# Performance work log

Measured on AMD Instinct MI355X. Metric: run time of the kernel, lower is better.

The kernel has to match this reference:

```python
import jax, jax.numpy as jnp
import numpy as np

B, L, D_IN, H, C = 64, 2048, 400, 200, 32
NEG = 1e12


def setup_inputs() -> dict:
    key = jax.random.key(0)
    k1, k2, k3, k4, k5 = jax.random.split(key, 5)
    x = jax.random.normal(k1, (B, L, D_IN), dtype=jnp.float32)
    category_bias = jax.random.normal(k2, (B, L, C), dtype=jnp.float32)
    att_mask = (jax.random.uniform(k3, (B, L)) > 0.2).astype(jnp.float32)
    # glorot-uniform-ish scales
    W_proj = jax.random.normal(k4, (D_IN, H), dtype=jnp.float32) * np.float32(np.sqrt(2.0 / (D_IN + H)))
    context = jax.random.normal(k5, (C, H), dtype=jnp.float32) * np.float32(np.sqrt(2.0 / (C + H)))
    lamada = jnp.zeros((1,), dtype=jnp.float32)
    return {"x": x, "category_bias": category_bias, "att_mask": att_mask,
            "W_proj": W_proj, "context": context, "lamada": lamada}


def reference(x, category_bias, att_mask, W_proj, context, lamada):
    # proj: [B, L, H] = tanh(x @ W_proj)  (Dense, no bias)
    proj = jnp.tanh(jnp.einsum("bld,dh->blh", x, W_proj))
    # scores vs learned context vectors: [B, L, C]
    weights = jnp.einsum("blh,ch->blc", proj, context) + lamada * category_bias
    # [B, C, L]
    weights = jnp.transpose(weights, (0, 2, 1))
    # additive large-negative mask, then softmax over sequence
    weights = weights - (1.0 - att_mask[:, None, :]) * NEG
    weights = jax.nn.softmax(weights, axis=-1)
    # poly representation: [B, C, D_IN]
    return jnp.einsum("bcl,bld->bcd", weights, x)
```

## Files before the change

kernel.cpp:

```cpp
#include <hip/hip_runtime.h>
#include <cmath>
#include <cstdint>

#define B_ 64
#define L_ 2048
#define DIN 400
#define H_ 200
#define C_ 32
#define NEGBIG 1e12f
#define KC1 13
#define NT1 13
#define KC2 7
#define MT2 2
#define NLC 8

typedef _Float16 half8 __attribute__((ext_vector_type(8)));
typedef float f32x4 __attribute__((ext_vector_type(4)));
typedef unsigned int uint4v __attribute__((ext_vector_type(4)));

__device__ __align__(16) _Float16 g_wfrag[KC1 * NT1 * 512];
__device__ __align__(16) _Float16 g_cfrag[KC2 * MT2 * 512];

static __device__ __forceinline__ f32x4 mfma16(half8 a, half8 b, f32x4 c) {
  return __builtin_amdgcn_mfma_f32_16x16x32_f16(a, b, c, 0, 0, 0);
}

static __device__ __forceinline__ float fast_tanh(float v) {
  const float e = __expf(2.0f * v);
  return 1.0f - 2.0f / (e + 1.0f);
}

__global__ __launch_bounds__(64) void k_prep(const float* __restrict__ Wp,
                                             const float* __restrict__ ctx)
{
  const int lane = threadIdx.x;
  const int bid = blockIdx.x;
  if (bid < KC1 * NT1) {
    const int q = bid / NT1, nt = bid % NT1;
    const int kb = q * 32 + (lane >> 4) * 8;
    const int n  = nt * 16 + (lane & 15);
    half8 h;
#pragma unroll
    for (int j = 0; j < 8; ++j) {
      const int k = kb + j;
      const float v = (k < DIN && n < H_) ? Wp[(size_t)k * H_ + n] : 0.0f;
      h[j] = (_Float16)v;
    }
    *reinterpret_cast<half8*>(&g_wfrag[((size_t)bid << 9) + (lane << 3)]) = h;
  } else {
    const int r = bid - KC1 * NT1;
    const int c  = (r % MT2) * 16 + (lane & 15);
    const int hb = (r / MT2) * 32 + (lane >> 4) * 8;
    half8 h;
#pragma unroll
    for (int j = 0; j < 8; ++j) {
      const int hh = hb + j;
      const float v = (hh < H_) ? ctx[(size_t)c * H_ + hh] : 0.0f;
      h[j] = (_Float16)v;
    }
    *reinterpret_cast<half8*>(&g_cfrag[((size_t)r << 9) + (lane << 3)]) = h;
  }
}

__global__ __launch_bounds__(256, 4) void k_scores(
    const float* __restrict__ x,
    const float* __restrict__ cb,
    const float* __restrict__ mask,
    const float* __restrict__ lam,
    float* __restrict__ S)
{
  __shared__ half8 smemv[1792];

  const int tid  = threadIdx.x;
  const int lane = tid & 63;
  const int w    = __builtin_amdgcn_readfirstlane(tid >> 6);
  const int b    = blockIdx.y;
  const int l0   = blockIdx.x * 64;
  const int oct  = lane >> 4;

  f32x4 acc[NT1];
#pragma unroll
  for (int nt = 0; nt < NT1; ++nt) acc[nt] = f32x4{0.f, 0.f, 0.f, 0.f};

  const float* xrow =
      x + ((size_t)b * L_ + l0 + w * 16 + (lane & 15)) * DIN + oct * 8;

  for (int i = w; i < NT1; i += 4) {
    const _Float16* gp = g_wfrag + (((size_t)i) << 9) + (lane << 3);
    __builtin_amdgcn_global_load_lds(
        (const __attribute__((address_space(1))) void*)gp,
        (__attribute__((address_space(3))) void*)(smemv + i * 64),
        16, 0, 0);
  }
  __builtin_amdgcn_sched_barrier(0);
  float4 cur0 = *reinterpret_cast<const float4*>(xrow);
  float4 cur1 = *reinterpret_cast<const float4*>(xrow + 4);

#pragma unroll
  for (int q = 0; q < KC1; ++q) {
    asm volatile("s_waitcnt vmcnt(2)\n\ts_barrier" ::: "memory");

    float4 nx0 = float4{0.f, 0.f, 0.f, 0.f};
    float4 nx1 = float4{0.f, 0.f, 0.f, 0.f};
    if (q < KC1 - 1) {
      const int nb = ((q + 1) & 1) * 832;
      for (int i = w; i < NT1; i += 4) {
        const _Float16* gp =
            g_wfrag + (((size_t)((q + 1) * NT1 + i)) << 9) + (lane << 3);
        __builtin_amdgcn_global_load_lds(
            (const __attribute__((address_space(1))) void*)gp,
            (__attribute__((address_space(3))) void*)(smemv + nb + i * 64),
            16, 0, 0);
      }
      __builtin_amdgcn_sched_barrier(0);
      const int k0 = (q + 1) * 32 + oct * 8;
      if (k0 + 7 < DIN) {
        nx0 = *reinterpret_cast<const float4*>(xrow + (q + 1) * 32);
        nx1 = *reinterpret_cast<const float4*>(xrow + (q + 1) * 32 + 4);
      }
    }

    float fa[8] = {cur0.x, cur0.y, cur0.z, cur0.w,
                   cur1.x, cur1.y, cur1.z, cur1.w};
    half8 ah, al;
#pragma unroll
    for (int j = 0; j < 8; ++j) {
      const _Float16 h = (_Float16)fa[j];
      ah[j] = h;
      al[j] = (_Float16)(fa[j] - (float)h);
    }

    const int base = (q & 1) * 832;
#pragma unroll
    for (int nt = 0; nt < NT1; ++nt) {
      const half8 bh = smemv[base + nt * 64 + lane];
      acc[nt] = mfma16(ah, bh, acc[nt]);
      acc[nt] = mfma16(al, bh, acc[nt]);
    }
    cur0 = nx0;
    cur1 = nx1;
  }

  __syncthreads();
  if (lane >= 32) {
    half8 z = {};
    smemv[(24 + w) * 64 + lane] = z;
  }
  _Float16* Pp = reinterpret_cast<_Float16*>(smemv);
#pragma unroll
  for (int nt = 0; nt < NT1; ++nt) {
    const int h   = nt * 16 + (lane & 15);
    const int q2  = h >> 5;
    const int lpw = ((h >> 3) & 3) << 4;
    const int jj  = h & 7;
#pragma unroll
    for (int reg = 0; reg < 4; ++reg) {
      const int t = ((lane >> 4) << 2) + reg;
      const float p = fast_tanh(acc[nt][reg]);
      Pp[(size_t)(((q2 * 4 + w) * 64) + lpw + t) * 8 + jj] = (_Float16)p;
    }
  }

  f32x4 s0 = f32x4{0.f, 0.f, 0.f, 0.f};
  f32x4 s1 = f32x4{0.f, 0.f, 0.f, 0.f};
#pragma unroll
  for (int q2 = 0; q2 < KC2; ++q2) {
    const half8 pb = smemv[(q2 * 4 + w) * 64 + lane];
    const half8 c0 = *reinterpret_cast<const half8*>(
        g_cfrag + (((size_t)(q2 * 2)) << 9) + (lane << 3));
    const half8 c1 = *reinterpret_cast<const half8*>(
        g_cfrag + (((size_t)(q2 * 2 + 1)) << 9) + (lane << 3));
    s0 = mfma16(c0, pb, s0);
    s1 = mfma16(c1, pb, s1);
  }

  const int tok = (w << 4) | (lane & 15);
  const size_t bl = (size_t)b * L_ + l0 + tok;
  const float lamv = lam[0];
  const float mk = (1.0f - mask[bl]) * NEGBIG;
  const int cq = (lane >> 4) << 2;
  const float4 cb0 = *reinterpret_cast<const float4*>(cb + bl * C_ + cq);
  const float4 cb1 = *reinterpret_cast<const float4*>(cb + bl * C_ + 16 + cq);
  float* Sp = S + (size_t)b * C_ * L_ + l0 + tok;
  Sp[(size_t)(cq + 0) * L_] = s0[0] + lamv * cb0.x - mk;
  Sp[(size_t)(cq + 1) * L_] = s0[1] + lamv * cb0.y - mk;
  Sp[(size_t)(cq + 2) * L_] = s0[2] + lamv * cb0.z - mk;
  Sp[(size_t)(cq + 3) * L_] = s0[3] + lamv * cb0.w - mk;
  Sp[(size_t)(16 + cq + 0) * L_] = s1[0] + lamv * cb1.x - mk;
  Sp[(size_t)(16 + cq + 1) * L_] = s1[1] + lamv * cb1.y - mk;
  Sp[(size_t)(16 + cq + 2) * L_] = s1[2] + lamv * cb1.z - mk;
  Sp[(size_t)(16 + cq + 3) * L_] = s1[3] + lamv * cb1.w - mk;
}

__global__ __launch_bounds__(256) void k_softmax(float* __restrict__ S,
                                                 _Float16* __restrict__ wh)
{
  const int row = blockIdx.x;
  float* R = S + (size_t)row * L_;
  const int tid = threadIdx.x;

  float v[8];
  float m = -3.4e38f;
#pragma unroll
  for (int j = 0; j < 8; ++j) {
    v[j] = R[tid + 256 * j];
    m = fmaxf(m, v[j]);
  }
#pragma unroll
  for (int o = 32; o > 0; o >>= 1) m = fmaxf(m, __shfl_xor(m, o));

  __shared__ float red[4];
  const int wid = tid >> 6;
  if ((tid & 63) == 0) red[wid] = m;
  __syncthreads();
  m = fmaxf(fmaxf(red[0], red[1]), fmaxf(red[2], red[3]));
  __syncthreads();

  float s = 0.f;
#pragma unroll
  for (int j = 0; j < 8; ++j) {
    v[j] = __expf(v[j] - m);
    s += v[j];
  }
#pragma unroll
  for (int o = 32; o > 0; o >>= 1) s += __shfl_xor(s, o);
  if ((tid & 63) == 0) red[wid] = s;
  __syncthreads();
  s = red[0] + red[1] + red[2] + red[3];

  const float inv = 1.0f / s;
  if (wh != nullptr) {
    _Float16* whr = wh + (size_t)row * L_;
#pragma unroll
    for (int j = 0; j < 8; ++j)
      whr[tid + 256 * j] = (_Float16)(v[j] * inv);
  } else {
#pragma unroll
    for (int j = 0; j < 8; ++j) R[tid + 256 * j] = v[j] * inv;
  }
}

__global__ __launch_bounds__(512, 4) void k_out_mfma(
    const float* __restrict__ x,
    const _Float16* __restrict__ wh,
    float* __restrict__ part)
{
  __shared__ unsigned int xsw[400 * 20];
  __shared__ unsigned int ws16[32][16];

  const int tid  = threadIdx.x;
  const int lane = tid & 63;
  const int w    = __builtin_amdgcn_readfirstlane(tid >> 6);
  const int b    = blockIdx.y;
  const int kq   = blockIdx.x;
  const int l0b  = kq * (L_ / NLC);

  const int ntile0 = (w < 7) ? w * 3 : 21;
  const int NTW    = (w < 7) ? 3 : 4;

  const int n   = lane & 15;
  const int oct = lane >> 4;

  f32x4 acc[4][2];
#pragma unroll
  for (int i = 0; i < 4; ++i) {
    acc[i][0] = f32x4{0.f, 0.f, 0.f, 0.f};
    acc[i][1] = f32x4{0.f, 0.f, 0.f, 0.f};
  }

  const float* xb = x + ((size_t)b * L_ + l0b) * DIN;
  const unsigned int* whb = reinterpret_cast<const unsigned int*>(
      wh + (size_t)b * C_ * L_ + l0b);

  const int lp0 = tid / 100 * 0;
  (void)lp0;

  float4 r0[4], r1[4];
  unsigned int wreg;

#pragma unroll
  for (int s = 0; s < 4; ++s) {
    const int i = s * 512 + tid;
    if (s < 3 || i < 1600) {
      const int lp = i / 100, qd = i - lp * 100;
      const float* src = xb + (size_t)(2 * lp) * DIN + 4 * qd;
      r0[s] = *reinterpret_cast<const float4*>(src);
      r1[s] = *reinterpret_cast<const float4*>(src + DIN);
    }
  }
  wreg = whb[((size_t)(tid >> 4) * L_) / 2 + (tid & 15)];

  const int NCH = (L_ / NLC) / 32;
  for (int ch = 0; ch < NCH; ++ch) {
    __syncthreads();

#pragma unroll
    for (int s = 0; s < 4; ++s) {
      const int i = s * 512 + tid;
      if (s < 3 || i < 1600) {
        const int lp = i / 100, qd = i - lp * 100;
#pragma unroll
        for (int k = 0; k < 4; ++k) {
          const int d = 4 * qd + k;
          const int sw = ((d >> 2) ^ (d >> 4)) & 3;
          const int col = (((lp >> 2) ^ sw) << 2) | (lp & 3);
          const _Float16 h0 = (_Float16)r0[s][k];
          const _Float16 h1 = (_Float16)r1[s][k];
          unsigned int pk = (unsigned int)__builtin_bit_cast(unsigned short, h0) |
                            ((unsigned int)__builtin_bit_cast(unsigned short, h1) << 16);
          xsw[d * 20 + col] = pk;
        }
      }
    }
    ws16[tid >> 4][tid & 15] = wreg;
    __syncthreads();

    if (ch + 1 < NCH) {
      const float* xc = xb + (size_t)((ch + 1) * 32) * DIN;
#pragma unroll
      for (int s = 0; s < 4; ++s) {
        const int i = s * 512 + tid;
        if (s < 3 || i < 1600) {
          const int lp = i / 100, qd = i - lp * 100;
          const float* src = xc + (size_t)(2 * lp) * DIN + 4 * qd;
          r0[s] = *reinterpret_cast<const float4*>(src);
          r1[s] = *reinterpret_cast<const float4*>(src + DIN);
        }
      }
      wreg = whb[((size_t)(tid >> 4) * L_ + (ch + 1) * 32) / 2 + (tid & 15)];
    }

    union { uint4v u; half8 h; } a0c, a1c;
    a0c.u = *reinterpret_cast<const uint4v*>(&ws16[n][oct * 4]);
    a1c.u = *reinterpret_cast<const uint4v*>(&ws16[n + 16][oct * 4]);
    const half8 a0 = a0c.h;
    const half8 a1 = a1c.h;

#pragma unroll
    for (int nt = 0; nt < 4; ++nt) {
      if (nt < NTW) {
        const int d0 = (ntile0 + nt) * 16 + n;
        const int sw = ((d0 >> 2) ^ (d0 >> 4)) & 3;
        const half8 bh = *reinterpret_cast<const half8*>(
            &xsw[d0 * 20 + ((oct ^ sw) << 2)]);
        acc[nt][0] = mfma16(a0, bh, acc[nt][0]);
        acc[nt][1] = mfma16(a1, bh, acc[nt][1]);
      }
    }
  }

  float* pb = part + ((size_t)(b * NLC + kq) * C_) * DIN;
#pragma unroll
  for (int nt = 0; nt < 4; ++nt) {
    if (nt < NTW) {
      const int d = (ntile0 + nt) * 16 + n;
#pragma unroll
      for (int mt = 0; mt < 2; ++mt) {
#pragma unroll
        for (int reg = 0; reg < 4; ++reg) {
          const int c = mt * 16 + oct * 4 + reg;
          pb[(size_t)c * DIN + d] = acc[nt][mt][reg];
        }
      }
    }
  }
}

__global__ __launch_bounds__(256) void k_out_reduce(
    const float* __restrict__ part, float* __restrict__ out)
{
  const int idx = blockIdx.x * 256 + threadIdx.x;
  const int b = idx / (C_ * DIN / 4);
  const int r = idx - b * (C_ * DIN / 4);
  const float4* p = reinterpret_cast<const float4*>(part) +
                    (size_t)b * NLC * (C_ * DIN / 4) + r;
  float4 s = float4{0.f, 0.f, 0.f, 0.f};
#pragma unroll
  for (int lc = 0; lc < NLC; ++lc) {
    const float4 v = p[(size_t)lc * (C_ * DIN / 4)];
    s.x += v.x; s.y += v.y; s.z += v.z; s.w += v.w;
  }
  reinterpret_cast<float4*>(out)[idx] = s;
}

__global__ __launch_bounds__(256) void k_out_atomic(
    const float* __restrict__ x,
    const float* __restrict__ Wt,
    float* __restrict__ out)
{
  __shared__ float ws_s[C_][256];
  const int tid  = threadIdx.x;
  const int b    = blockIdx.y;
  const int lc0  = blockIdx.x * 256;
  const int g    = __builtin_amdgcn_readfirstlane(tid >> 6);
  const int lane = tid & 63;

  {
    const int c  = tid >> 3;
    const int lb = (tid & 7) * 32;
    const float* src = Wt + ((size_t)b * C_ + c) * L_ + lc0 + lb;
#pragma unroll
    for (int j = 0; j < 32; j += 4)
      *reinterpret_cast<float4*>(&ws_s[c][lb + j]) =
          *reinterpret_cast<const float4*>(src + j);
  }
  __syncthreads();

  float a1[8][4] = {};
  float a2[8][4] = {};
  const bool has2 = lane < 36;
  const float* xb = x + ((size_t)b * L_ + lc0) * DIN;
  const int d1 = lane * 4;
  const int d2 = 256 + lane * 4;

  for (int l = 0; l < 256; ++l) {
    const float4 xv = *reinterpret_cast<const float4*>(xb + (size_t)l * DIN + d1);
    float4 xv2 = float4{0.f, 0.f, 0.f, 0.f};
    if (has2) xv2 = *reinterpret_cast<const float4*>(xb + (size_t)l * DIN + d2);
#pragma unroll
    for (int i = 0; i < 8; ++i) {
      const float wv = ws_s[g * 8 + i][l];
      a1[i][0] = fmaf(wv, xv.x, a1[i][0]);
      a1[i][1] = fmaf(wv, xv.y, a1[i][1]);
      a1[i][2] = fmaf(wv, xv.z, a1[i][2]);
      a1[i][3] = fmaf(wv, xv.w, a1[i][3]);
      a2[i][0] = fmaf(wv, xv2.x, a2[i][0]);
      a2[i][1] = fmaf(wv, xv2.y, a2[i][1]);
      a2[i][2] = fmaf(wv, xv2.z, a2[i][2]);
      a2[i][3] = fmaf(wv, xv2.w, a2[i][3]);
    }
  }

  float* ob = out + ((size_t)b * C_ + g * 8) * DIN;
#pragma unroll
  for (int i = 0; i < 8; ++i) {
#pragma unroll
    for (int kk = 0; kk < 4; ++kk)
      atomicAdd(ob + (size_t)i * DIN + d1 + kk, a1[i][kk]);
    if (has2) {
#pragma unroll
      for (int kk = 0; kk < 4; ++kk)
        atomicAdd(ob + (size_t)i * DIN + d2 + kk, a2[i][kk]);
    }
  }
}

extern "C" void kernel_launch(void* const* d_in, const int* in_sizes, int n_in,
                              void* d_out, int out_size, void* d_ws, size_t ws_size,
                              hipStream_t stream)
{
  const float* x    = (const float*)d_in[0];
  const float* cb   = (const float*)d_in[1];
  const float* mask = (const float*)d_in[2];
  const float* Wp   = (const float*)d_in[3];
  const float* ctx  = (const float*)d_in[4];
  const float* lam  = (const float*)d_in[5];
  float* out = (float*)d_out;

  const size_t part_elems = (size_t)B_ * NLC * C_ * DIN;
  float* wsf  = (float*)d_ws;
  float* S    = wsf;
  float* part = wsf;
  _Float16* wh = (_Float16*)(wsf + part_elems);
  const size_t need = part_elems * sizeof(float) +
                      (size_t)B_ * C_ * L_ * sizeof(_Float16);

  k_prep<<<dim3(KC1 * NT1 + KC2 * MT2), 64, 0, stream>>>(Wp, ctx);
  k_scores<<<dim3(L_ / 64, B_), 256, 0, stream>>>(x, cb, mask, lam, S);

  if (ws_size >= need) {
    k_softmax<<<dim3(B_ * C_), 256, 0, stream>>>(S, wh);
    k_out_mfma<<<dim3(NLC, B_), 512, 0, stream>>>(x, wh, part);
    k_out_reduce<<<dim3(B_ * C_ * DIN / 4 / 256), 256, 0, stream>>>(part, out);
  } else {
    k_softmax<<<dim3(B_ * C_), 256, 0, stream>>>(S, nullptr);
    hipMemsetAsync(d_out, 0, (size_t)out_size * sizeof(float), stream);
    k_out_atomic<<<dim3(L_ / 256, B_), 256, 0, stream>>>(x, S, out);
  }
}
```

Baseline: 116.3 us.

## Give each k_scores wave two row tiles to reuse W fragments

```diff
diff --git a/kernel.cpp b/kernel.cpp
--- a/kernel.cpp
+++ b/kernel.cpp
@@ -62,7 +62,7 @@
   }
 }
 
-__global__ __launch_bounds__(256, 4) void k_scores(
+__global__ __launch_bounds__(128, 2) void k_scores(
     const float* __restrict__ x,
     const float* __restrict__ cb,
     const float* __restrict__ mask,
@@ -78,14 +78,17 @@
   const int l0   = blockIdx.x * 64;
   const int oct  = lane >> 4;
 
-  f32x4 acc[NT1];
-#pragma unroll
-  for (int nt = 0; nt < NT1; ++nt) acc[nt] = f32x4{0.f, 0.f, 0.f, 0.f};
-
-  const float* xrow =
-      x + ((size_t)b * L_ + l0 + w * 16 + (lane & 15)) * DIN + oct * 8;
-
-  for (int i = w; i < NT1; i += 4) {
+  f32x4 acc[2][NT1];
+#pragma unroll
+  for (int mt = 0; mt < 2; ++mt)
+#pragma unroll
+    for (int nt = 0; nt < NT1; ++nt) acc[mt][nt] = f32x4{0.f, 0.f, 0.f, 0.f};
+
+  const float* xrow0 =
+      x + ((size_t)b * L_ + l0 + w * 32 + (lane & 15)) * DIN + oct * 8;
+  const float* xrow1 = xrow0 + (size_t)16 * DIN;
+
+  for (int i = w; i < NT1; i += 2) {
     const _Float16* gp = g_wfrag + (((size_t)i) << 9) + (lane << 3);
     __builtin_amdgcn_global_load_lds(
         (const __attribute__((address_space(1))) void*)gp,
@@ -93,18 +96,22 @@
         16, 0, 0);
   }
   __builtin_amdgcn_sched_barrier(0);
-  float4 cur0 = *reinterpret_cast<const float4*>(xrow);
-  float4 cur1 = *reinterpret_cast<const float4*>(xrow + 4);
+  float4 c00 = *reinterpret_cast<const float4*>(xrow0);
+  float4 c01 = *reinterpret_cast<const float4*>(xrow0 + 4);
+  float4 c10 = *reinterpret_cast<const float4*>(xrow1);
+  float4 c11 = *reinterpret_cast<const float4*>(xrow1 + 4);
 
 #pragma unroll
   for (int q = 0; q < KC1; ++q) {
-    asm volatile("s_waitcnt vmcnt(2)\n\ts_barrier" ::: "memory");
-
-    float4 nx0 = float4{0.f, 0.f, 0.f, 0.f};
-    float4 nx1 = float4{0.f, 0.f, 0.f, 0.f};
+    asm volatile("s_waitcnt vmcnt(4)\n\ts_barrier" ::: "memory");
+
+    float4 n00 = float4{0.f, 0.f, 0.f, 0.f};
+    float4 n01 = float4{0.f, 0.f, 0.f, 0.f};
+    float4 n10 = float4{0.f, 0.f, 0.f, 0.f};
+    float4 n11 = float4{0.f, 0.f, 0.f, 0.f};
     if (q < KC1 - 1) {
       const int nb = ((q + 1) & 1) * 832;
-      for (int i = w; i < NT1; i += 4) {
+      for (int i = w; i < NT1; i += 2) {
         const _Float16* gp =
             g_wfrag + (((size_t)((q + 1) * NT1 + i)) << 9) + (lane << 3);
         __builtin_amdgcn_global_load_lds(
@@ -115,81 +122,102 @@
       __builtin_amdgcn_sched_barrier(0);
       const int k0 = (q + 1) * 32 + oct * 8;
       if (k0 + 7 < DIN) {
-        nx0 = *reinterpret_cast<const float4*>(xrow + (q + 1) * 32);
-        nx1 = *reinterpret_cast<const float4*>(xrow + (q + 1) * 32 + 4);
-      }
-    }
-
-    float fa[8] = {cur0.x, cur0.y, cur0.z, cur0.w,
-                   cur1.x, cur1.y, cur1.z, cur1.w};
-    half8 ah, al;
+        n00 = *reinterpret_cast<const float4*>(xrow0 + (q + 1) * 32);
+        n01 = *reinterpret_cast<const float4*>(xrow0 + (q + 1) * 32 + 4);
+        n10 = *reinterpret_cast<const float4*>(xrow1 + (q + 1) * 32);
+        n11 = *reinterpret_cast<const float4*>(xrow1 + (q + 1) * 32 + 4);
+      }
+    }
+
+    float fa0[8] = {c00.x, c00.y, c00.z, c00.w, c01.x, c01.y, c01.z, c01.w};
+    float fa1[8] = {c10.x, c10.y, c10.z, c10.w, c11.x, c11.y, c11.z, c11.w};
+    half8 ah0, al0, ah1, al1;
 #pragma unroll
     for (int j = 0; j < 8; ++j) {
-      const _Float16 h = (_Float16)fa[j];
-      ah[j] = h;
-      al[j] = (_Float16)(fa[j] - (float)h);
+      const _Float16 h0 = (_Float16)fa0[j];
+      ah0[j] = h0;
+      al0[j] = (_Float16)(fa0[j] - (float)h0);
+      const _Float16 h1 = (_Float16)fa1[j];
+      ah1[j] = h1;
+      al1[j] = (_Float16)(fa1[j] - (float)h1);
     }
 
     const int base = (q & 1) * 832;
 #pragma unroll
     for (int nt = 0; nt < NT1; ++nt) {
       const half8 bh = smemv[base + nt * 64 + lane];
-      acc[nt] = mfma16(ah, bh, acc[nt]);
-      acc[nt] = mfma16(al, bh, acc[nt]);
-    }
-    cur0 = nx0;
-    cur1 = nx1;
+      acc[0][nt] = mfma16(ah0, bh, acc[0][nt]);
+      acc[0][nt] = mfma16(al0, bh, acc[0][nt]);
+      acc[1][nt] = mfma16(ah1, bh, acc[1][nt]);
+      acc[1][nt] = mfma16(al1, bh, acc[1][nt]);
+    }
+    c00 = n00; c01 = n01; c10 = n10; c11 = n11;
   }
 
   __syncthreads();
   if (lane >= 32) {
     half8 z = {};
-    smemv[(24 + w) * 64 + lane] = z;
+    smemv[(24 + w * 2 + 0) * 64 + lane] = z;
+    smemv[(24 + w * 2 + 1) * 64 + lane] = z;
   }
   _Float16* Pp = reinterpret_cast<_Float16*>(smemv);
 #pragma unroll
-  for (int nt = 0; nt < NT1; ++nt) {
-    const int h   = nt * 16 + (lane & 15);
-    const int q2  = h >> 5;
-    const int lpw = ((h >> 3) & 3) << 4;
-    const int jj  = h & 7;
-#pragma unroll
-    for (int reg = 0; reg < 4; ++reg) {
-      const int t = ((lane >> 4) << 2) + reg;
-      const float p = fast_tanh(acc[nt][reg]);
-      Pp[(size_t)(((q2 * 4 + w) * 64) + lpw + t) * 8 + jj] = (_Float16)p;
-    }
-  }
-
-  f32x4 s0 = f32x4{0.f, 0.f, 0.f, 0.f};
-  f32x4 s1 = f32x4{0.f, 0.f, 0.f, 0.f};
+  for (int mt = 0; mt < 2; ++mt) {
+    const int tile = w * 2 + mt;
+#pragma unroll
+    for (int nt = 0; nt < NT1; ++nt) {
+      const int h   = nt * 16 + (lane & 15);
+      const int q2  = h >> 5;
+      const int lpw = ((h >> 3) & 3) << 4;
+      const int jj  = h & 7;
+#pragma unroll
+      for (int reg = 0; reg < 4; ++reg) {
+        const int t = ((lane >> 4) << 2) + reg;
+        const float p = fast_tanh(acc[mt][nt][reg]);
+        Pp[(size_t)(((q2 * 4 + tile) * 64) + lpw + t) * 8 + jj] = (_Float16)p;
+      }
+    }
+  }
+
+  f32x4 s[2][2];
+#pragma unroll
+  for (int mt = 0; mt < 2; ++mt) {
+    s[mt][0] = f32x4{0.f, 0.f, 0.f, 0.f};
+    s[mt][1] = f32x4{0.f, 0.f, 0.f, 0.f};
+  }
 #pragma unroll
   for (int q2 = 0; q2 < KC2; ++q2) {
-    const half8 pb = smemv[(q2 * 4 + w) * 64 + lane];
-    const half8 c0 = *reinterpret_cast<const half8*>(
+    const half8 cf0 = *reinterpret_cast<const half8*>(
         g_cfrag + (((size_t)(q2 * 2)) << 9) + (lane << 3));
-    const half8 c1 = *reinterpret_cast<const half8*>(
+    const half8 cf1 = *reinterpret_cast<const half8*>(
         g_cfrag + (((size_t)(q2 * 2 + 1)) << 9) + (lane << 3));
-    s0 = mfma16(c0, pb, s0);
-    s1 = mfma16(c1, pb, s1);
-  }
-
-  const int tok = (w << 4) | (lane & 15);
-  const size_t bl = (size_t)b * L_ + l0 + tok;
+#pragma unroll
+    for (int mt = 0; mt < 2; ++mt) {
+      const half8 pb = smemv[(q2 * 4 + w * 2 + mt) * 64 + lane];
+      s[mt][0] = mfma16(cf0, pb, s[mt][0]);
+      s[mt][1] = mfma16(cf1, pb, s[mt][1]);
+    }
+  }
+
   const float lamv = lam[0];
-  const float mk = (1.0f - mask[bl]) * NEGBIG;
   const int cq = (lane >> 4) << 2;
-  const float4 cb0 = *reinterpret_cast<const float4*>(cb + bl * C_ + cq);
-  const float4 cb1 = *reinterpret_cast<const float4*>(cb + bl * C_ + 16 + cq);
-  float* Sp = S + (size_t)b * C_ * L_ + l0 + tok;
-  Sp[(size_t)(cq + 0) * L_] = s0[0] + lamv * cb0.x - mk;
-  Sp[(size_t)(cq + 1) * L_] = s0[1] + lamv * cb0.y - mk;
-  Sp[(size_t)(cq + 2) * L_] = s0[2] + lamv * cb0.z - mk;
-  Sp[(size_t)(cq + 3) * L_] = s0[3] + lamv * cb0.w - mk;
-  Sp[(size_t)(16 + cq + 0) * L_] = s1[0] + lamv * cb1.x - mk;
-  Sp[(size_t)(16 + cq + 1) * L_] = s1[1] + lamv * cb1.y - mk;
-  Sp[(size_t)(16 + cq + 2) * L_] = s1[2] + lamv * cb1.z - mk;
-  Sp[(size_t)(16 + cq + 3) * L_] = s1[3] + lamv * cb1.w - mk;
+#pragma unroll
+  for (int mt = 0; mt < 2; ++mt) {
+    const int tok = (w * 2 + mt) * 16 + (lane & 15);
+    const size_t bl = (size_t)b * L_ + l0 + tok;
+    const float mk = (1.0f - mask[bl]) * NEGBIG;
+    const float4 cb0 = *reinterpret_cast<const float4*>(cb + bl * C_ + cq);
+    const float4 cb1 = *reinterpret_cast<const float4*>(cb + bl * C_ + 16 + cq);
+    float* Sp = S + (size_t)b * C_ * L_ + l0 + tok;
+    Sp[(size_t)(cq + 0) * L_] = s[mt][0][0] + lamv * cb0.x - mk;
+    Sp[(size_t)(cq + 1) * L_] = s[mt][0][1] + lamv * cb0.y - mk;
+    Sp[(size_t)(cq + 2) * L_] = s[mt][0][2] + lamv * cb0.z - mk;
+    Sp[(size_t)(cq + 3) * L_] = s[mt][0][3] + lamv * cb0.w - mk;
+    Sp[(size_t)(16 + cq + 0) * L_] = s[mt][1][0] + lamv * cb1.x - mk;
+    Sp[(size_t)(16 + cq + 1) * L_] = s[mt][1][1] + lamv * cb1.y - mk;
+    Sp[(size_t)(16 + cq + 2) * L_] = s[mt][1][2] + lamv * cb1.z - mk;
+    Sp[(size_t)(16 + cq + 3) * L_] = s[mt][1][3] + lamv * cb1.w - mk;
+  }
 }
 
 __global__ __launch_bounds__(256) void k_softmax(float* __restrict__ S,
@@ -271,9 +299,6 @@
   const float* xb = x + ((size_t)b * L_ + l0b) * DIN;
   const unsigned int* whb = reinterpret_cast<const unsigned int*>(
       wh + (size_t)b * C_ * L_ + l0b);
-
-  const int lp0 = tid / 100 * 0;
-  (void)lp0;
 
   float4 r0[4], r1[4];
   unsigned int wreg;
@@ -466,7 +491,7 @@
                       (size_t)B_ * C_ * L_ * sizeof(_Float16);
 
   k_prep<<<dim3(KC1 * NT1 + KC2 * MT2), 64, 0, stream>>>(Wp, ctx);
-  k_scores<<<dim3(L_ / 64, B_), 256, 0, stream>>>(x, cb, mask, lam, S);
+  k_scores<<<dim3(L_ / 64, B_), 128, 0, stream>>>(x, cb, mask, lam, S);
 
   if (ws_size >= need) {
     k_softmax<<<dim3(B_ * C_), 256, 0, stream>>>(S, wh);
```

New measurement: 118.9 us. +2.3%, slower.
